# Kernel tuning notes

Measured on AMD Instinct MI355X. Metric: run time of the kernel, lower is better.

The kernel has to match this reference:

```python
import jax, jax.numpy as jnp
import numpy as np

B, L, C = 32, 1024, 32     # batch, seq_len, enc_in
D = 512                     # d_model / hidden_size
SEG = 16                    # seg_len
K = 25                      # moving_avg kernel
SX = L // SEG               # seg_num_x = 64 sequential GRU steps
PRED = 16                   # pred_len == seg_len -> seg_num_y = 1


def setup_inputs() -> dict:
    key = jax.random.key(0)
    ks = jax.random.split(key, 20)
    r = lambda i, shape: jax.random.normal(ks[i], shape, dtype=jnp.float32) * 0.05
    return {
        "x": jax.random.normal(ks[0], (B, L, C), dtype=jnp.float32),
        "W_emb": r(1, (D, SEG)), "b_emb": r(2, (D,)),
        "Wih_s": r(3, (3 * D, D)), "Whh_s": r(4, (3 * D, D)),
        "bih_s": r(5, (3 * D,)), "bhh_s": r(6, (3 * D,)),
        "Wih_t": r(7, (3 * D, D)), "Whh_t": r(8, (3 * D, D)),
        "bih_t": r(9, (3 * D,)), "bhh_t": r(10, (3 * D,)),
        "pos_s": r(11, (1, D // 2)), "ch_s": r(12, (C, D // 2)),
        "pos_t": r(13, (1, D // 2)), "ch_t": r(14, (C, D // 2)),
        "Wps": r(15, (SEG, D)), "bps": r(16, (SEG,)),
        "Wpt": r(17, (SEG, D)), "bpt": r(18, (SEG,)),
    }


def _moving_mean(x, k):
    # Autoformer moving_avg over dim 1 with edge replication (length preserved, k odd)
    pad = (k - 1) // 2
    xp = jnp.concatenate([jnp.repeat(x[:, :1], pad, 1), x, jnp.repeat(x[:, -1:], pad, 1)], axis=1)
    cs = jnp.cumsum(xp, axis=1)
    cs = jnp.concatenate([jnp.zeros_like(cs[:, :1]), cs], axis=1)
    return (cs[:, k:] - cs[:, :-k]) / k


def _gru_cell(x, h, Wih, Whh, bih, bhh):
    gi = x @ Wih.T + bih
    gh = h @ Whh.T + bhh
    ir, iz, in_ = jnp.split(gi, 3, axis=-1)
    hr, hz, hn = jnp.split(gh, 3, axis=-1)
    r = jax.nn.sigmoid(ir + hr)
    z = jax.nn.sigmoid(iz + hz)
    n = jnp.tanh(in_ + r * hn)
    return (1.0 - z) * n + z * h


def _forward(x, W_emb, b_emb, Wih_s, Whh_s, bih_s, bhh_s, Wih_t, Whh_t, bih_t, bhh_t,
             pos_s, ch_s, pos_t, ch_t, Wps, bps, Wpt, bpt):
    seq_last = jax.lax.stop_gradient(x[:, -1:, :])          # (B,1,C), detached
    xc = (x - seq_last).transpose(0, 2, 1)                  # (B,C,L)
    mean = _moving_mean(xc, K)                              # trend
    xs = xc - mean                                          # seasonal residual
    xt = mean
    # value embedding: (B*C, SX, SEG) -> (B*C, SX, D), ReLU
    xs = jax.nn.relu(xs.reshape(-1, SX, SEG) @ W_emb.T + b_emb)
    xt = jax.nn.relu(xt.reshape(-1, SX, SEG) @ W_emb.T + b_emb)
    N = B * C
    h0 = jnp.zeros((N, D), x.dtype)

    def step(carry, inp):
        hs, ht = carry
        xs_i, xt_i = inp
        hs = _gru_cell(xs_i, hs, Wih_s, Whh_s, bih_s, bhh_s)
        ht = _gru_cell(xt_i, ht, Wih_t, Whh_t, bih_t, bhh_t)
        return (hs, ht), None

    (hs, ht), _ = jax.lax.scan(step, (h0, h0), (xs.transpose(1, 0, 2), xt.transpose(1, 0, 2)))

    # decoder (seg_num_y == 1): pos/channel embedding -> one more GRUCell step
    pe_s = jnp.tile(jnp.concatenate([jnp.broadcast_to(pos_s, (C, D // 2)), ch_s], -1), (B, 1))  # (B*C,D)
    pe_t = jnp.tile(jnp.concatenate([jnp.broadcast_to(pos_t, (C, D // 2)), ch_t], -1), (B, 1))
    hs2 = _gru_cell(pe_s, hs, Wih_s, Whh_s, bih_s, bhh_s)
    ht2 = _gru_cell(pe_t, ht, Wih_t, Whh_t, bih_t, bhh_t)
    # predict heads (dropout is identity in eval)
    y = ht2 @ Wpt.T + bpt + hs2 @ Wps.T + bps               # (B*C, SEG)
    y = y.reshape(B, C, PRED).transpose(0, 2, 1)            # (B, PRED, C)
    return y + seq_last


def reference(x, W_emb, b_emb, Wih_s, Whh_s, bih_s, bhh_s, Wih_t, Whh_t, bih_t, bhh_t,
              pos_s, ch_s, pos_t, ch_t, Wps, bps, Wpt, bpt):
    return _forward(x, W_emb, b_emb, Wih_s, Whh_s, bih_s, bhh_s, Wih_t, Whh_t, bih_t, bhh_t,
                    pos_s, ch_s, pos_t, ch_t, Wps, bps, Wpt, bpt)
```

## Files before the change

kernel.cpp:

```cpp
#include <hip/hip_runtime.h>
#include <math.h>

#define B_   32
#define L_   1024
#define C_   32
#define D_   512
#define SEG_ 16
#define SX_  64
#define N_   1024

typedef _Float16 f16x8 __attribute__((ext_vector_type(8)));
typedef _Float16 f16x4 __attribute__((ext_vector_type(4)));
typedef float    f32x4 __attribute__((ext_vector_type(4)));

__device__ __forceinline__ void stage16(const void* g, void* l) {
    __builtin_amdgcn_global_load_lds((const __attribute__((address_space(1))) void*)g,
                                     (__attribute__((address_space(3))) void*)l, 16, 0, 0);
}
__device__ __forceinline__ void stage16l(const void* g, void* l) {
    __builtin_amdgcn_global_load_lds((const __attribute__((address_space(1))) void*)g,
                                     (__attribute__((address_space(3))) void*)l, 16, 0, 1);
}
__device__ __forceinline__ void store_v4_sc0(void* p, f16x8 v) {
    asm volatile("global_store_dwordx4 %0, %1, off sc0" :: "v"(p), "v"(v) : "memory");
}
__device__ __forceinline__ float fsig(float x) {
    return __builtin_amdgcn_rcpf(1.f + __expf(-x));
}
__device__ __forceinline__ float ftanh(float x) {
    return 1.f - 2.f * __builtin_amdgcn_rcpf(1.f + __expf(2.f * x));
}

__global__ __launch_bounds__(256) void setup_kernel(
    const float* __restrict__ x, float* __restrict__ xs_seg, float* __restrict__ xt_seg,
    const float* __restrict__ Wih_s, const float* __restrict__ Wih_t,
    _Float16* __restrict__ wih_pk,
    const float* __restrict__ Whh_s, const float* __restrict__ Whh_t,
    _Float16* __restrict__ whh_pk5,
    const float* __restrict__ pos_s, const float* __restrict__ ch_s,
    const float* __restrict__ pos_t, const float* __restrict__ ch_t,
    _Float16* __restrict__ pe) {
    int bid = blockIdx.x, tid = threadIdx.x;
    if (bid < 6144) {
        int e = bid * 256 + tid;
        int kk = e & 31;
        int t = e >> 5;
        int gc = t % 1536;
        int t2 = t / 1536;
        int kt = t2 & 15, gru = t2 >> 4;
        int member = gc / 192, r = gc % 192;
        int wn = r / 48, r2 = r % 48;
        int gate = r2 >> 4, jl = r2 & 15;
        int j = member * 64 + wn * 16 + jl;
        int k = kt * 32 + kk;
        const float* W = gru ? Wih_t : Wih_s;
        wih_pk[e] = (_Float16)W[(size_t)(gate * 512 + j) * 512 + k];
    } else if (bid < 12288) {
        int e = (bid - 6144) * 256 + tid;
        int fi = e & 7;
        int t = e >> 3;
        int c = t % 3072;
        int t2 = t / 3072;
        int kt = t2 & 3;
        int t3 = t2 >> 2;
        int member = t3 & 7, gru = t3 >> 3;
        int gc = c >> 4, s = c & 15;
        int q = s ^ (gc & 15);
        int k = kt * 128 + q * 8 + fi;
        int wn = gc / 48, r2 = gc % 48;
        int gate = r2 >> 4, jl = r2 & 15;
        int j = member * 64 + wn * 16 + jl;
        const float* W = gru ? Whh_t : Whh_s;
        whh_pk5[e] = (_Float16)W[(size_t)(gate * 512 + j) * 512 + k];
    } else if (bid < 16384) {
        int e = (bid - 12288) * 256 + tid;
        int k = e & 511;
        int n = (e >> 9) & 1023;
        int gru = e >> 19;
        int c = n & 31;
        const float* pos = gru ? pos_t : pos_s;
        const float* ch  = gru ? ch_t  : ch_s;
        float v = (k < 256) ? pos[k] : ch[c * 256 + (k - 256)];
        pe[e] = (_Float16)v;
    } else {
        int b2 = bid - 16384;
        int b = b2 >> 2;
        int t = ((b2 & 3) << 8) + tid;
        const float* xb    = x + (size_t)b * (L_ * C_);
        const float* xrow  = xb + (size_t)t * C_;
        const float* xlast = xb + (size_t)(L_ - 1) * C_;
        float diff[C_];
#pragma unroll
        for (int c = 0; c < C_; ++c) diff[c] = xrow[c] - xlast[c];
        float ps[C_ + 1];
        ps[0] = 0.f;
#pragma unroll
        for (int c = 0; c < C_; ++c) ps[c + 1] = ps[c] + diff[c];
        int s = t >> 4, q = t & 15;
#pragma unroll
        for (int c = 0; c < C_; ++c) {
            int lo = c - 12, hi = c + 12;
            float sum = ps[(hi < 31 ? hi : 31) + 1] - ps[lo > 0 ? lo : 0];
            if (lo < 0)  sum += (float)(-lo)     * diff[0];
            if (hi > 31) sum += (float)(hi - 31) * diff[31];
            float mean = sum * (1.0f / 25.0f);
            size_t idx = ((size_t)s * N_ + (size_t)(b * C_ + c)) * SEG_ + q;
            xt_seg[idx] = mean;
            xs_seg[idx] = diff[c] - mean;
        }
    }
}

__global__ __launch_bounds__(256) void emb_kernel(
    const float* __restrict__ xs_seg, const float* __restrict__ xt_seg,
    const float* __restrict__ W_emb, const float* __restrict__ b_emb,
    _Float16* __restrict__ emb_buf, int s0) {
    int bid = blockIdx.x;
    int gru = bid >> 8, sl = (bid >> 4) & 15, nch = bid & 15;
    int step = s0 + sl, n0 = nch * 64;
    const float* xseg = gru ? xt_seg : xs_seg;
    __shared__ float xl[64 * 16];
    int tid = threadIdx.x;
    const float* src = xseg + ((size_t)step * N_ + n0) * SEG_;
    for (int i = tid; i < 1024; i += 256) xl[i] = src[i];

    int kg = tid & 127;
    int rh = tid >> 7;
    float w[4][16], bb[4];
#pragma unroll
    for (int i = 0; i < 4; ++i) {
        int k = kg * 4 + i;
        const float4* wr = (const float4*)(W_emb + (size_t)k * 16);
#pragma unroll
        for (int v = 0; v < 4; ++v) {
            float4 tt = wr[v];
            w[i][v * 4 + 0] = tt.x; w[i][v * 4 + 1] = tt.y;
            w[i][v * 4 + 2] = tt.z; w[i][v * 4 + 3] = tt.w;
        }
        bb[i] = b_emb[k];
    }
    __syncthreads();
    _Float16* dst = emb_buf + ((size_t)(sl * 2 + gru) * N_ + n0) * D_ + kg * 4;
    for (int r = 0; r < 32; ++r) {
        int row = rh * 32 + r;
        float a0 = bb[0], a1 = bb[1], a2 = bb[2], a3 = bb[3];
#pragma unroll
        for (int q = 0; q < 16; ++q) {
            float xv = xl[row * 16 + q];
            a0 = fmaf(xv, w[0][q], a0);
            a1 = fmaf(xv, w[1][q], a1);
            a2 = fmaf(xv, w[2][q], a2);
            a3 = fmaf(xv, w[3][q], a3);
        }
        f16x4 v;
        v[0] = (_Float16)(a0 > 0.f ? a0 : 0.f);
        v[1] = (_Float16)(a1 > 0.f ? a1 : 0.f);
        v[2] = (_Float16)(a2 > 0.f ? a2 : 0.f);
        v[3] = (_Float16)(a3 > 0.f ? a3 : 0.f);
        *(f16x4*)(dst + (size_t)row * D_) = v;
    }
}

__global__ __launch_bounds__(512, 2) void gi_gemm_kernel(
    const _Float16* __restrict__ emb, const _Float16* __restrict__ pe,
    const _Float16* __restrict__ wih_pack,
    _Float16* __restrict__ gi, _Float16* __restrict__ gi_pe, int mode) {
    __shared__ __align__(16) char smem[53248];
    char* sA = smem;
    char* sB = smem + 8192;
    int Nt = blockIdx.x & 7, Mt = blockIdx.x >> 3;
    int sl = blockIdx.y, gru = blockIdx.z;
    int tid = threadIdx.x, w = tid >> 6, lane = tid & 63;
    int wm = w & 1, wn = w >> 1, ml = lane & 15, qq = lane >> 4;

    const char* Ab = mode ? (const char*)(pe  + (size_t)gru * N_ * D_)
                          : (const char*)(emb + (size_t)(sl * 2 + gru) * N_ * D_);
    const char* Bb = (const char*)wih_pack + (size_t)gru * 16 * 1536 * 64
                     + (size_t)Nt * 192 * 64;

    int rA = tid >> 2, kqA = (tid & 3) ^ ((rA >> 1) & 3);
    const char* gA = Ab + (size_t)(Mt * 128 + rA) * 1024 + kqA * 16;
    int g1 = tid >> 2, kq1 = (tid & 3) ^ ((g1 >> 1) & 3);
    int c2 = 512 + tid, g2 = c2 >> 2, kq2 = (c2 & 3) ^ ((g2 >> 1) & 3);

    int offA[4], offB[3];
#pragma unroll
    for (int mf = 0; mf < 4; ++mf) {
        int row = wm * 64 + mf * 16 + ml;
        offA[mf] = (row * 4 + (qq ^ ((row >> 1) & 3))) * 16;
    }
#pragma unroll
    for (int g = 0; g < 3; ++g) {
        int gc = wn * 48 + g * 16 + ml;
        offB[g] = (gc * 4 + (qq ^ ((gc >> 1) & 3))) * 16;
    }

    f32x4 acc[4][3];
#pragma unroll
    for (int mf = 0; mf < 4; ++mf)
#pragma unroll
        for (int g = 0; g < 3; ++g) {
            f32x4 z = {0.f, 0.f, 0.f, 0.f};
            acc[mf][g] = z;
        }

    for (int kt = 0; kt < 16; ++kt) {
        __syncthreads();
        stage16(gA + kt * 64, sA + w * 1024);
        const char* Bkt = Bb + (size_t)kt * (1536 * 64);
        stage16(Bkt + g1 * 64 + kq1 * 16, sB + w * 1024);
        if (w < 4) stage16(Bkt + g2 * 64 + kq2 * 16, sB + 8192 + w * 1024);
        asm volatile("s_waitcnt vmcnt(0)" ::: "memory");
        __syncthreads();
        f16x8 a[4];
#pragma unroll
        for (int mf = 0; mf < 4; ++mf) a[mf] = *(const f16x8*)(sA + offA[mf]);
#pragma unroll
        for (int g = 0; g < 3; ++g) {
            f16x8 b = *(const f16x8*)(sB + offB[g]);
#pragma unroll
            for (int mf = 0; mf < 4; ++mf)
                acc[mf][g] = __builtin_amdgcn_mfma_f32_16x16x32_f16(a[mf], b, acc[mf][g], 0, 0, 0);
        }
    }

    __syncthreads();
#pragma unroll
    for (int mf = 0; mf < 4; ++mf) {
        int wm_c = mf >> 1, rt = mf & 1;
        int tid_c = (wn * 2 + wm_c) * 64 + qq * 16 + ml;
        char* base = smem + wm * 26624 + tid_c * 52;
#pragma unroll
        for (int g = 0; g < 3; ++g)
#pragma unroll
            for (int reg = 0; reg < 4; ++reg) {
                int v = rt * 12 + reg * 3 + g;
                *(_Float16*)(base + v * 2) = (_Float16)acc[mf][g][reg];
            }
    }
    __syncthreads();
    _Float16* ob = mode ? gi_pe + (size_t)gru * 8 * 16 * 512 * 24
                        : gi    + (size_t)(sl * 2 + gru) * 8 * 16 * 512 * 24;
    char* obB = (char*)ob;
#pragma unroll
    for (int s = 0; s < 6; ++s) {
        int o = tid * 16 + s * 8192;
        int mc = o / 24576;
        int o2 = o - mc * 24576;
        int tc = o2 / 48;
        int r  = o2 - tc * 48;
        const char* src = smem + mc * 26624 + tc * 52 + r;
        int4 val;
        val.x = *(const int*)(src);
        val.y = *(const int*)(src + 4);
        val.z = *(const int*)(src + 8);
        val.w = *(const int*)(src + 12);
        *(int4*)(obB + (size_t)(Nt * 16 + Mt * 2 + mc) * 24576 + o2) = val;
    }
}

__global__ __launch_bounds__(512) void gru_chain_kernel(
    const _Float16* __restrict__ whh_pk5,
    const _Float16* __restrict__ gi_base,
    const float* __restrict__ bih_s, const float* __restrict__ bhh_s,
    const float* __restrict__ bih_t, const float* __restrict__ bhh_t,
    _Float16* __restrict__ hbf0, _Float16* __restrict__ hbf1,
    unsigned* __restrict__ flags, int nsteps, int sbase) {
    __shared__ __align__(16) char smem[65536];
    char* sA = smem;
    char* sEx = smem + 16384;
    int bid = blockIdx.x;
    int member = bid >> 5, chain = bid & 31;
    int Mt = chain & 15, gru = chain >> 4;
    int tid = threadIdx.x, w = tid >> 6, lane = tid & 63;
    int ml = lane & 15, qq = lane >> 4;
    int km = w & 1, wn = w >> 1;

    const char* h0 = (const char*)hbf0 + ((size_t)gru * N_ + Mt * 64) * 1024;
    const char* h1 = (const char*)hbf1 + ((size_t)gru * N_ + Mt * 64) * 1024;

    f16x8 bfr[3][8];
    {
        const _Float16* Wb = whh_pk5 + (size_t)(gru * 8 + member) * 4 * 24576;
#pragma unroll
        for (int g = 0; g < 3; ++g) {
            int gc = wn * 48 + g * 16 + ml;
#pragma unroll
            for (int ks = 0; ks < 8; ++ks) {
                int kt = km * 2 + (ks >> 2);
                int q8 = ((ks & 3) * 4 + qq) ^ (gc & 15);
                bfr[g][ks] = *(const f16x8*)(Wb + (size_t)kt * 24576
                                             + (size_t)(gc * 16 + q8) * 8);
            }
        }
    }

    int cS0 = (lane & 48) | ((lane & 15) ^ (w & 15));
    int cS1 = (lane & 48) | ((lane & 15) ^ ((w + 8) & 15));

    int offR[4], cp[8];
#pragma unroll
    for (int rt = 0; rt < 4; ++rt) offR[rt] = (rt * 16 + ml) * 1024;
#pragma unroll
    for (int ks = 0; ks < 8; ++ks) {
        int c = km * 32 + ks * 4 + qq;
        cp[ks] = ((c & 48) | ((c & 15) ^ ml)) * 16;
    }

    const float* bi = gru ? bih_t : bih_s;
    const float* bh = gru ? bhh_t : bhh_s;
    int j = member * 64 + wn * 16 + ml;
    float bir = bi[j], biz = bi[D_ + j], bin = bi[2 * D_ + j];
    float bhr = bh[j], bhz = bh[D_ + j], bhn = bh[2 * D_ + j];
    float hp[2][4];
#pragma unroll
    for (int rtL = 0; rtL < 2; ++rtL)
#pragma unroll
        for (int reg = 0; reg < 4; ++reg) {
            int row = Mt * 64 + km * 32 + rtL * 16 + qq * 4 + reg;
            hp[rtL][reg] = (float)hbf0[((size_t)gru * N_ + row) * D_ + j];
        }

    unsigned* fbase = flags + chain * 256;
    const _Float16* giTid0 = gi_base
        + (((size_t)gru * 8 + member) * 16 + Mt) * 512 * 24 + (size_t)tid * 24;
    size_t giStep = (size_t)2 * 8 * 16 * 512 * 24;

    int dir0 = sbase & 1;
    f16x8 gv0, gv1, gv2;
    {
        const _Float16* gp = giTid0;
        gv0 = *(const f16x8*)(gp);
        gv1 = *(const f16x8*)(gp + 8);
        gv2 = *(const f16x8*)(gp + 16);
        const char* hin = dir0 ? h1 : h0;
#pragma unroll
        for (int r = 0; r < 8; ++r) {
            int row = r * 8 + w;
            stage16l(hin + (size_t)row * 1024 + (size_t)((r & 1) ? cS1 : cS0) * 16,
                     sA + row * 1024);
        }
    }

    for (int it = 0; it < nsteps; ++it) {
        int gstep = sbase + it;
        _Float16* hout = (gstep & 1) ? hbf0 : hbf1;

        f32x4 acc[4][3];
#pragma unroll
        for (int rt = 0; rt < 4; ++rt)
#pragma unroll
            for (int g = 0; g < 3; ++g) {
                f32x4 z = {0.f, 0.f, 0.f, 0.f};
                acc[rt][g] = z;
            }

        asm volatile("s_waitcnt vmcnt(0)" ::: "memory");
        __syncthreads();

        int itn = (it + 1 < nsteps) ? it + 1 : it;
        const _Float16* gpn = giTid0 + (size_t)itn * giStep;
        f16x8 ngv0 = *(const f16x8*)(gpn);
        f16x8 ngv1 = *(const f16x8*)(gpn + 8);
        f16x8 ngv2 = *(const f16x8*)(gpn + 16);
        __builtin_amdgcn_sched_barrier(0);

#pragma unroll
        for (int ks = 0; ks < 8; ++ks) {
            f16x8 a0 = *(const f16x8*)(sA + offR[0] + cp[ks]);
            f16x8 a1 = *(const f16x8*)(sA + offR[1] + cp[ks]);
            f16x8 a2 = *(const f16x8*)(sA + offR[2] + cp[ks]);
            f16x8 a3 = *(const f16x8*)(sA + offR[3] + cp[ks]);
#pragma unroll
            for (int g = 0; g < 3; ++g) {
                acc[0][g] = __builtin_amdgcn_mfma_f32_16x16x32_f16(a0, bfr[g][ks], acc[0][g], 0, 0, 0);
                acc[1][g] = __builtin_amdgcn_mfma_f32_16x16x32_f16(a1, bfr[g][ks], acc[1][g], 0, 0, 0);
                acc[2][g] = __builtin_amdgcn_mfma_f32_16x16x32_f16(a2, bfr[g][ks], acc[2][g], 0, 0, 0);
                acc[3][g] = __builtin_amdgcn_mfma_f32_16x16x32_f16(a3, bfr[g][ks], acc[3][g], 0, 0, 0);
            }
        }

        __syncthreads();
        char* exw = sEx + (size_t)(wn * 64 + lane) * 16;
        if (km == 0) {
#pragma unroll
            for (int g = 0; g < 3; ++g) {
                *(f32x4*)(exw + (size_t)(6 + g) * 4096) = acc[2][g];
                *(f32x4*)(exw + (size_t)(9 + g) * 4096) = acc[3][g];
            }
        } else {
#pragma unroll
            for (int g = 0; g < 3; ++g) {
                *(f32x4*)(exw + (size_t)(0 + g) * 4096) = acc[0][g];
                *(f32x4*)(exw + (size_t)(3 + g) * 4096) = acc[1][g];
            }
        }
        __syncthreads();
        f32x4 s0[3], s1[3];
        if (km == 0) {
#pragma unroll
            for (int g = 0; g < 3; ++g) {
                s0[g] = acc[0][g] + *(const f32x4*)(exw + (size_t)(0 + g) * 4096);
                s1[g] = acc[1][g] + *(const f32x4*)(exw + (size_t)(3 + g) * 4096);
            }
        } else {
#pragma unroll
            for (int g = 0; g < 3; ++g) {
                s0[g] = acc[2][g] + *(const f32x4*)(exw + (size_t)(6 + g) * 4096);
                s1[g] = acc[3][g] + *(const f32x4*)(exw + (size_t)(9 + g) * 4096);
            }
        }

        char* sH = sA;
        int colb = (wn * 16 + ml) * 2;
#pragma unroll
        for (int reg = 0; reg < 4; ++reg) {
            int v0 = reg * 3;
            float gr = (float)((v0 + 0) < 8 ? gv0[(v0 + 0) & 7]
                      : ((v0 + 0) < 16 ? gv1[(v0 + 0) & 7] : gv2[(v0 + 0) & 7]));
            float gz = (float)((v0 + 1) < 8 ? gv0[(v0 + 1) & 7]
                      : ((v0 + 1) < 16 ? gv1[(v0 + 1) & 7] : gv2[(v0 + 1) & 7]));
            float gn = (float)((v0 + 2) < 8 ? gv0[(v0 + 2) & 7]
                      : ((v0 + 2) < 16 ? gv1[(v0 + 2) & 7] : gv2[(v0 + 2) & 7]));
            float r = fsig(s0[0][reg] + gr + bir + bhr);
            float z = fsig(s0[1][reg] + gz + biz + bhz);
            float nn = ftanh(gn + bin + r * (s0[2][reg] + bhn));
            float hv = (1.f - z) * nn + z * hp[0][reg];
            hp[0][reg] = hv;
            int rl = km * 32 + qq * 4 + reg;
            *(_Float16*)(sH + rl * 144 + colb) = (_Float16)hv;
        }
#pragma unroll
        for (int reg = 0; reg < 4; ++reg) {
            int v0 = 12 + reg * 3;
            float gr = (float)((v0 + 0) < 8 ? gv0[(v0 + 0) & 7]
                      : ((v0 + 0) < 16 ? gv1[(v0 + 0) & 7] : gv2[(v0 + 0) & 7]));
            float gz = (float)((v0 + 1) < 8 ? gv0[(v0 + 1) & 7]
                      : ((v0 + 1) < 16 ? gv1[(v0 + 1) & 7] : gv2[(v0 + 1) & 7]));
            float gn = (float)((v0 + 2) < 8 ? gv0[(v0 + 2) & 7]
                      : ((v0 + 2) < 16 ? gv1[(v0 + 2) & 7] : gv2[(v0 + 2) & 7]));
            float r = fsig(s1[0][reg] + gr + bir + bhr);
            float z = fsig(s1[1][reg] + gz + biz + bhz);
            float nn = ftanh(gn + bin + r * (s1[2][reg] + bhn));
            float hv = (1.f - z) * nn + z * hp[1][reg];
            hp[1][reg] = hv;
            int rl = km * 32 + 16 + qq * 4 + reg;
            *(_Float16*)(sH + rl * 144 + colb) = (_Float16)hv;
        }
        __syncthreads();
        {
            int srow = tid >> 3, spart = tid & 7;
            f16x8 hv8 = *(const f16x8*)(sH + srow * 144 + spart * 16);
            _Float16* gdst = hout + ((size_t)gru * N_ + Mt * 64 + srow) * D_
                             + member * 64 + spart * 8;
            store_v4_sc0(gdst, hv8);
        }

        asm volatile("s_waitcnt vmcnt(0)" ::: "memory");
        __syncthreads();
        if (tid == 0)
            __hip_atomic_store(fbase + member * 32, (unsigned)(gstep + 1),
                               __ATOMIC_RELAXED, __HIP_MEMORY_SCOPE_AGENT);

        if (it < nsteps - 1) {
            if (w == 0) {
                const unsigned* fp = fbase + (lane & 7) * 32;
                unsigned tgt = (unsigned)(gstep + 1);
                int guard = 0;
                while (true) {
                    unsigned v = __hip_atomic_load(fp, __ATOMIC_RELAXED,
                                                   __HIP_MEMORY_SCOPE_AGENT);
                    if (__all(v >= tgt)) break;
                    __builtin_amdgcn_s_sleep(1);
                    if (++guard > (1 << 20)) break;
                }
            }
            __syncthreads();
            const char* hinN = ((gstep + 1) & 1) ? h1 : h0;
#pragma unroll
            for (int r = 0; r < 8; ++r) {
                int row = r * 8 + w;
                stage16l(hinN + (size_t)row * 1024 + (size_t)((r & 1) ? cS1 : cS0) * 16,
                         sA + row * 1024);
            }
        }
        gv0 = ngv0; gv1 = ngv1; gv2 = ngv2;
    }
}

__global__ __launch_bounds__(256) void head_kernel(
    const _Float16* __restrict__ hs2, const _Float16* __restrict__ ht2,
    const float* __restrict__ Wps, const float* __restrict__ bps,
    const float* __restrict__ Wpt, const float* __restrict__ bpt,
    const float* __restrict__ x, float* __restrict__ out) {
    int g = blockIdx.x * 256 + threadIdx.x;
    int n = g >> 4, p = g & 15;
    int b = n >> 5, c = n & 31;
    const _Float16* hs = hs2 + (size_t)n * D_;
    const _Float16* ht = ht2 + (size_t)n * D_;
    const float* ws = Wps + (size_t)p * D_;
    const float* wt = Wpt + (size_t)p * D_;
    float acc = bps[p] + bpt[p];
    for (int k = 0; k < D_; ++k)
        acc += (float)hs[k] * ws[k] + (float)ht[k] * wt[k];
    float last = x[((size_t)b * L_ + (L_ - 1)) * C_ + c];
    out[((size_t)b * SEG_ + p) * C_ + c] = acc + last;
}

extern "C" void kernel_launch(void* const* d_in, const int* in_sizes, int n_in,
                              void* d_out, int out_size, void* d_ws, size_t ws_size,
                              hipStream_t stream) {
    const float* x     = (const float*)d_in[0];
    const float* W_emb = (const float*)d_in[1];
    const float* b_emb = (const float*)d_in[2];
    const float* Wih_s = (const float*)d_in[3];
    const float* Whh_s = (const float*)d_in[4];
    const float* bih_s = (const float*)d_in[5];
    const float* bhh_s = (const float*)d_in[6];
    const float* Wih_t = (const float*)d_in[7];
    const float* Whh_t = (const float*)d_in[8];
    const float* bih_t = (const float*)d_in[9];
    const float* bhh_t = (const float*)d_in[10];
    const float* pos_s = (const float*)d_in[11];
    const float* ch_s  = (const float*)d_in[12];
    const float* pos_t = (const float*)d_in[13];
    const float* ch_t  = (const float*)d_in[14];
    const float* Wps   = (const float*)d_in[15];
    const float* bps   = (const float*)d_in[16];
    const float* Wpt   = (const float*)d_in[17];
    const float* bpt   = (const float*)d_in[18];
    float* out = (float*)d_out;

    char* p = (char*)d_ws;
    float* xs_seg = (float*)p;          p += (size_t)SX_ * N_ * SEG_ * 4;
    float* xt_seg = (float*)p;          p += (size_t)SX_ * N_ * SEG_ * 4;
    _Float16* emb_buf = (_Float16*)p;   p += (size_t)16 * 2 * N_ * D_ * 2;
    _Float16* gi_buf  = (_Float16*)p;   p += (size_t)16 * 2 * 8 * 16 * 512 * 24 * 2;
    _Float16* gi_pe   = (_Float16*)p;   p += (size_t)2 * 8 * 16 * 512 * 24 * 2;
    _Float16* pe_buf  = (_Float16*)p;   p += (size_t)2 * N_ * D_ * 2;
    _Float16* wih_pk  = (_Float16*)p;   p += (size_t)2 * 16 * 1536 * 32 * 2;
    _Float16* whh_pk5 = (_Float16*)p;   p += (size_t)2 * 8 * 4 * 3072 * 8 * 2;
    _Float16* hbf0 = (_Float16*)p;      p += (size_t)2 * N_ * D_ * 2;
    _Float16* hbf1 = (_Float16*)p;      p += (size_t)2 * N_ * D_ * 2;
    unsigned* flags = (unsigned*)p;     p += 32 * 256 * 4;

    hipMemsetAsync(hbf0, 0, (size_t)2 * N_ * D_ * 2, stream);
    hipMemsetAsync(flags, 0, 32 * 256 * 4, stream);

    setup_kernel<<<16512, 256, 0, stream>>>(
        x, xs_seg, xt_seg, Wih_s, Wih_t, wih_pk, Whh_s, Whh_t, whh_pk5,
        pos_s, ch_s, pos_t, ch_t, pe_buf);

    for (int b = 0; b < 4; ++b) {
        emb_kernel<<<512, 256, 0, stream>>>(xs_seg, xt_seg, W_emb, b_emb, emb_buf, b * 16);
        gi_gemm_kernel<<<dim3(64, 16, 2), 512, 0, stream>>>(
            emb_buf, pe_buf, wih_pk, gi_buf, gi_pe, 0);
        gru_chain_kernel<<<256, 512, 0, stream>>>(
            whh_pk5, gi_buf, bih_s, bhh_s, bih_t, bhh_t,
            hbf0, hbf1, flags, 16, b * 16);
    }
    gi_gemm_kernel<<<dim3(64, 1, 2), 512, 0, stream>>>(
        emb_buf, pe_buf, wih_pk, gi_buf, gi_pe, 1);
    gru_chain_kernel<<<256, 512, 0, stream>>>(
        whh_pk5, gi_pe, bih_s, bhh_s, bih_t, bhh_t,
        hbf0, hbf1, flags, 1, 64);

    head_kernel<<<N_ * SEG_ / 256, 256, 0, stream>>>(
        hbf1, hbf1 + (size_t)N_ * D_, Wps, bps, Wpt, bpt, x, out);
}
```

Measured before the change: 809.9 us.

## Double K-tile per stage in gi GEMM and split GRU exchange buffer

The input-gate GEMM now stages 128-wide K slices (two 64-element halves) per iteration with a new 8-way XOR swizzle. That halves the number of barrier/wait rounds from 16 to 8 and issues more loads per round. In the GRU chain kernel, the exchange area is moved into its own shared array separate from the A buffer, which allows one __syncthreads before the exchange writes to be removed. The cost is more LDS per block: 115 KB in the chain kernel, and the GEMM's B region moved to offset 16384. This could reduce occupancy, and the address math of the new layout must be correct.

Result: no change. 819.4 us (+1.2%).

```diff
diff --git a/kernel.cpp b/kernel.cpp
--- a/kernel.cpp
+++ b/kernel.cpp
@@ -167,7 +167,7 @@
     _Float16* __restrict__ gi, _Float16* __restrict__ gi_pe, int mode) {
     __shared__ __align__(16) char smem[53248];
     char* sA = smem;
-    char* sB = smem + 8192;
+    char* sB = smem + 16384;
     int Nt = blockIdx.x & 7, Mt = blockIdx.x >> 3;
     int sl = blockIdx.y, gru = blockIdx.z;
     int tid = threadIdx.x, w = tid >> 6, lane = tid & 63;
@@ -178,22 +178,19 @@
     const char* Bb = (const char*)wih_pack + (size_t)gru * 16 * 1536 * 64
                      + (size_t)Nt * 192 * 64;
 
-    int rA = tid >> 2, kqA = (tid & 3) ^ ((rA >> 1) & 3);
-    const char* gA = Ab + (size_t)(Mt * 128 + rA) * 1024 + kqA * 16;
-    int g1 = tid >> 2, kq1 = (tid & 3) ^ ((g1 >> 1) & 3);
-    int c2 = 512 + tid, g2 = c2 >> 2, kq2 = (c2 & 3) ^ ((g2 >> 1) & 3);
-
+    int row0 = tid >> 3;
+    int sq = (tid & 7) ^ (row0 & 7);
+    const char* gA0 = Ab + (size_t)(Mt * 128 + row0) * 1024 + sq * 16;
+    const char* gA1 = gA0 + 65536;
+    size_t gBk = (size_t)(sq >> 2) * 98304 + (size_t)row0 * 64 + (size_t)(sq & 3) * 16;
+
+    int xq0 = (qq ^ (ml & 7)) * 16;
+    int xq1 = ((4 + qq) ^ (ml & 7)) * 16;
     int offA[4], offB[3];
 #pragma unroll
-    for (int mf = 0; mf < 4; ++mf) {
-        int row = wm * 64 + mf * 16 + ml;
-        offA[mf] = (row * 4 + (qq ^ ((row >> 1) & 3))) * 16;
-    }
-#pragma unroll
-    for (int g = 0; g < 3; ++g) {
-        int gc = wn * 48 + g * 16 + ml;
-        offB[g] = (gc * 4 + (qq ^ ((gc >> 1) & 3))) * 16;
-    }
+    for (int mf = 0; mf < 4; ++mf) offA[mf] = (wm * 64 + mf * 16 + ml) * 128;
+#pragma unroll
+    for (int g = 0; g < 3; ++g) offB[g] = (wn * 48 + g * 16 + ml) * 128;
 
     f32x4 acc[4][3];
 #pragma unroll
@@ -204,23 +201,32 @@
             acc[mf][g] = z;
         }
 
-    for (int kt = 0; kt < 16; ++kt) {
+    for (int s = 0; s < 8; ++s) {
         __syncthreads();
-        stage16(gA + kt * 64, sA + w * 1024);
-        const char* Bkt = Bb + (size_t)kt * (1536 * 64);
-        stage16(Bkt + g1 * 64 + kq1 * 16, sB + w * 1024);
-        if (w < 4) stage16(Bkt + g2 * 64 + kq2 * 16, sB + 8192 + w * 1024);
+        stage16(gA0 + s * 128, sA + w * 1024);
+        stage16(gA1 + s * 128, sA + 8192 + w * 1024);
+        const char* Bs = Bb + (size_t)s * 196608 + gBk;
+        stage16(Bs, sB + w * 1024);
+        stage16(Bs + 4096, sB + 8192 + w * 1024);
+        stage16(Bs + 8192, sB + 16384 + w * 1024);
         asm volatile("s_waitcnt vmcnt(0)" ::: "memory");
         __syncthreads();
-        f16x8 a[4];
-#pragma unroll
-        for (int mf = 0; mf < 4; ++mf) a[mf] = *(const f16x8*)(sA + offA[mf]);
+        f16x8 a0[4], a1[4];
+#pragma unroll
+        for (int mf = 0; mf < 4; ++mf) {
+            a0[mf] = *(const f16x8*)(sA + offA[mf] + xq0);
+            a1[mf] = *(const f16x8*)(sA + offA[mf] + xq1);
+        }
 #pragma unroll
         for (int g = 0; g < 3; ++g) {
-            f16x8 b = *(const f16x8*)(sB + offB[g]);
+            f16x8 b0 = *(const f16x8*)(sB + offB[g] + xq0);
 #pragma unroll
             for (int mf = 0; mf < 4; ++mf)
-                acc[mf][g] = __builtin_amdgcn_mfma_f32_16x16x32_f16(a[mf], b, acc[mf][g], 0, 0, 0);
+                acc[mf][g] = __builtin_amdgcn_mfma_f32_16x16x32_f16(a0[mf], b0, acc[mf][g], 0, 0, 0);
+            f16x8 b1 = *(const f16x8*)(sB + offB[g] + xq1);
+#pragma unroll
+            for (int mf = 0; mf < 4; ++mf)
+                acc[mf][g] = __builtin_amdgcn_mfma_f32_16x16x32_f16(a1[mf], b1, acc[mf][g], 0, 0, 0);
         }
     }
 
@@ -266,9 +272,8 @@
     const float* __restrict__ bih_t, const float* __restrict__ bhh_t,
     _Float16* __restrict__ hbf0, _Float16* __restrict__ hbf1,
     unsigned* __restrict__ flags, int nsteps, int sbase) {
-    __shared__ __align__(16) char smem[65536];
-    char* sA = smem;
-    char* sEx = smem + 16384;
+    __shared__ __align__(16) char sA[65536];
+    __shared__ __align__(16) char sEx[49152];
     int bid = blockIdx.x;
     int member = bid >> 5, chain = bid & 31;
     int Mt = chain & 15, gru = chain >> 4;
@@ -380,7 +385,6 @@
             }
         }
 
-        __syncthreads();
         char* exw = sEx + (size_t)(wn * 64 + lane) * 16;
         if (km == 0) {
 #pragma unroll
```
